# Optimization experiments

Measured on AMD Instinct MI355X. Metric: run time of the kernel, lower is better.

Reference implementation:

```python
import jax, jax.numpy as jnp
import numpy as np

B, L, C, H = 2, 4096, 512, 8
DH = C // H


def setup_inputs() -> dict:
    key = jax.random.key(0)
    ks = jax.random.split(key, 6)
    s = 1.0 / np.sqrt(C)
    return {
        "x": jax.random.normal(ks[0], (B, L, C), dtype=jnp.float32),
        "Wq": jax.random.normal(ks[1], (C, C), dtype=jnp.float32) * s,
        "Wk": jax.random.normal(ks[2], (C, C), dtype=jnp.float32) * s,
        "Wv": jax.random.normal(ks[3], (C, C), dtype=jnp.float32) * s,
        "Wo": jax.random.normal(ks[4], (C, C), dtype=jnp.float32) * s,
        "bo": jnp.zeros((C,), dtype=jnp.float32),
    }


def reference(x, Wq, Wk, Wv, Wo, bo):
    # x: [B, L, C]; split heads -> [B, H, L, Dh]
    def heads(t):
        return t.reshape(B, L, H, DH).transpose(0, 2, 1, 3)

    q = heads(x @ Wq)
    k = heads(x @ Wk)
    v = heads(x @ Wv)
    scale = 1.0 / np.sqrt(DH)
    scores = jnp.einsum("bhqd,bhkd->bhqk", q, k) * scale  # [B,H,L,L]
    w = jax.nn.softmax(scores, axis=-1)  # dropout_rate=0.0 -> identity
    att = jnp.einsum("bhqk,bhkd->bhqd", w, v)  # [B,H,L,Dh]
    att = att.transpose(0, 2, 1, 3).reshape(B, L, C)
    return att @ Wo + bo
```

## Files before the change

kernel.cpp:

```cpp
#include <hip/hip_runtime.h>
#include <hip/hip_bf16.h>

typedef __hip_bfloat16 bh;
typedef __attribute__((ext_vector_type(8))) __bf16 bf16x8;
typedef __attribute__((ext_vector_type(4))) float f32x4;
typedef __attribute__((ext_vector_type(4))) int i32x4;
typedef __attribute__((ext_vector_type(4))) short s16x4;

#define NB 2
#define NL 4096
#define NC 512
#define NH 8
#define NDH 64
#define NM (NB * NL)
#define LOG2E 1.4426950408889634f
#define KVBLK 8192

static __device__ __forceinline__ f32x4 mfma_bf16(bf16x8 a, bf16x8 b, f32x4 c) {
    return __builtin_amdgcn_mfma_f32_16x16x32_bf16(a, b, c, 0, 0, 0);
}

static __device__ __forceinline__ void st_bf4(bh* dst, float a, float b, float c, float d) {
    bh tmp[4] = {__float2bfloat16(a), __float2bfloat16(b),
                 __float2bfloat16(c), __float2bfloat16(d)};
    *(s16x4*)dst = *(const s16x4*)tmp;
}
static __device__ __forceinline__ bf16x8 pk_bf8(float a0, float a1, float a2, float a3,
                                                float b0, float b1, float b2, float b3) {
    bh tmp[8] = {__float2bfloat16(a0), __float2bfloat16(a1),
                 __float2bfloat16(a2), __float2bfloat16(a3),
                 __float2bfloat16(b0), __float2bfloat16(b1),
                 __float2bfloat16(b2), __float2bfloat16(b3)};
    return *(const bf16x8*)tmp;
}

static __device__ __forceinline__ void gload16(const bh* g, bh* l) {
    __builtin_amdgcn_global_load_lds(
        (const __attribute__((address_space(1))) void*)g,
        (__attribute__((address_space(3))) void*)l,
        16, 0, 0);
}

__global__ __launch_bounds__(256, 2)
void prep(const float* __restrict__ x,
          const float* __restrict__ Wq, const float* __restrict__ Wk,
          const float* __restrict__ Wv, const float* __restrict__ Wo,
          bh* __restrict__ xf, bh* __restrict__ Wf)
{
    const int t = threadIdx.x;
    const int wave = t >> 6, lane = t & 63;
    const int quad = lane >> 4, c16 = lane & 15;

    if (blockIdx.z < 8) {
        __shared__ __align__(16) bh T[64][72];
        const int m64 = blockIdx.x, k64 = blockIdx.z;
        #pragma unroll
        for (int rep = 0; rep < 4; rep++) {
            int li = t + rep * 256;
            int r = li >> 4, c4 = (li & 15) * 4;
            float4 f = *(const float4*)&x[(size_t)(m64 * 64 + r) * 512 + k64 * 64 + c4];
            st_bf4(&T[r][c4], f.x, f.y, f.z, f.w);
        }
        __syncthreads();
        #pragma unroll
        for (int kcl = 0; kcl < 2; kcl++) {
            i32x4 v = *(const i32x4*)&T[wave * 16 + c16][kcl * 32 + quad * 8];
            size_t addr = ((size_t)(m64 * 4 + wave) * 16 + (k64 * 2 + kcl)) * 512 + lane * 8;
            *(i32x4*)&xf[addr] = v;
        }
    } else {
        if (blockIdx.x >= 64) return;
        int task = blockIdx.x * 4 + wave;
        int z = task >> 6, nt = (task >> 3) & 7, k0i = task & 7;
        const float* W = (z == 0) ? Wq : (z == 1) ? Wk : (z == 2) ? Wv : Wo;
        bh* dst = Wf + (((size_t)z * 8 + nt) * 8 + k0i) * 4096;
        #pragma unroll
        for (int kc = 0; kc < 2; kc++)
            #pragma unroll
            for (int fn = 0; fn < 4; fn++) {
                bh tmp[8];
                #pragma unroll
                for (int j = 0; j < 8; j++)
                    tmp[j] = __float2bfloat16(
                        W[(size_t)(k0i * 64 + kc * 32 + quad * 8 + j) * 512
                          + nt * 64 + fn * 16 + c16]);
                *(i32x4*)&dst[(kc * 4 + fn) * 512 + lane * 8] = *(const i32x4*)tmp;
            }
    }
}

__global__ __launch_bounds__(256, 2)
void qkv_gemm(const bh* __restrict__ xf, const bh* __restrict__ Wf,
              bh* __restrict__ Qb, bh* __restrict__ KVf)
{
    __shared__ __align__(16) bh smem[2][20480];

    const int t = threadIdx.x;
    const int wave = t >> 6, lane = t & 63;
    const int quad = lane >> 4, c16 = lane & 15;
    const int m0 = blockIdx.x * 128;
    const int nt = blockIdx.y;
    const int m16b = m0 >> 4;

    f32x4 acc[3][2][4];
    for (int z = 0; z < 3; z++)
        for (int a = 0; a < 2; a++)
            for (int b = 0; b < 4; b++)
                for (int u = 0; u < 4; u++) acc[z][a][b][u] = 0.0f;

    auto stage = [&](int k0i, int buf) {
        bh* Xl = &smem[buf][0];
        bh* Wl = &smem[buf][8192];
        #pragma unroll
        for (int r = 0; r < 4; r++) {
            int f = wave * 4 + r;
            const bh* src = xf + ((size_t)(m16b + (f >> 1)) * 16 + k0i * 2 + (f & 1)) * 512
                          + lane * 8;
            gload16(src, &Xl[f * 512 + lane * 8]);
        }
        #pragma unroll
        for (int z = 0; z < 3; z++) {
            const bh* wz = Wf + (((size_t)z * 8 + nt) * 8 + k0i) * 4096;
            #pragma unroll
            for (int r = 0; r < 2; r++) {
                int off = (wave * 2 + r) * 512 + lane * 8;
                gload16(wz + off, &Wl[z * 4096 + off]);
            }
        }
    };

    stage(0, 0);
    for (int k0i = 0; k0i < 8; k0i++) {
        const int buf = k0i & 1;
        __syncthreads();
        if (k0i < 7) stage(k0i + 1, buf ^ 1);
        const bh* Xl = &smem[buf][0];
        const bh* Wl = &smem[buf][8192];
        #pragma unroll
        for (int kc = 0; kc < 2; kc++) {
            bf16x8 af0 = *(const bf16x8*)&Xl[((wave * 2 + 0) * 2 + kc) * 512 + lane * 8];
            bf16x8 af1 = *(const bf16x8*)&Xl[((wave * 2 + 1) * 2 + kc) * 512 + lane * 8];
            #pragma unroll
            for (int z = 0; z < 3; z++)
                #pragma unroll
                for (int fn = 0; fn < 4; fn++) {
                    bf16x8 bf = *(const bf16x8*)&Wl[z * 4096 + (kc * 4 + fn) * 512 + lane * 8];
                    acc[z][0][fn] = mfma_bf16(af0, bf, acc[z][0][fn]);
                    acc[z][1][fn] = mfma_bf16(af1, bf, acc[z][1][fn]);
                }
        }
        __syncthreads();
    }

    const int h = nt;
    const int b = m0 >> 12;
    const int l0 = m0 & 4095;
    const int bh_i = b * NH + h;
    const int kt0 = l0 >> 6;

    {
        bh* Tq = &smem[0][0];
        #pragma unroll
        for (int fm = 0; fm < 2; fm++)
            #pragma unroll
            for (int i = 0; i < 4; i++) {
                int ll = wave * 32 + fm * 16 + quad * 4 + i;
                #pragma unroll
                for (int fn = 0; fn < 4; fn++)
                    Tq[ll * 68 + fn * 16 + c16] =
                        __float2bfloat16(acc[0][fm][fn][i] * 0.125f);
            }
        __syncthreads();
        int l = t >> 1, half = t & 1;
        bh* dst = Qb + ((size_t)bh_i * NL + l0 + l) * NDH + half * 32;
        const bh* src = &Tq[l * 68 + half * 32];
        #pragma unroll
        for (int r = 0; r < 4; r++)
            *(i32x4*)(dst + r * 8) = *(const i32x4*)(src + r * 8);
        __syncthreads();
    }

    {
        bh* Tk = &smem[0][0];
        #pragma unroll
        for (int fm = 0; fm < 2; fm++)
            #pragma unroll
            for (int i = 0; i < 4; i++) {
                int ll = wave * 32 + fm * 16 + quad * 4 + i;
                int ktl = ll >> 6, l64 = ll & 63;
                int fk = l64 >> 4, c16t = l64 & 15;
                #pragma unroll
                for (int fn = 0; fn < 4; fn++) {
                    int d = fn * 16 + c16;
                    int kc = d >> 5, qt = (d >> 3) & 3, j = d & 7;
                    Tk[ktl * 4096 + (fk * 2 + kc) * 512 + (qt * 16 + c16t) * 8 + j] =
                        __float2bfloat16(acc[1][fm][fn][i] * LOG2E);
                }
            }
        __syncthreads();
        int idx = t * 32;
        int ktl = idx >> 12, wi = idx & 4095;
        bh* dst = KVf + (size_t)(bh_i * 64 + kt0 + ktl) * KVBLK + wi;
        #pragma unroll
        for (int r = 0; r < 4; r++)
            *(i32x4*)(dst + r * 8) = *(const i32x4*)&Tk[idx + r * 8];
    }

    #pragma unroll
    for (int fm = 0; fm < 2; fm++) {
        int fkv = (wave * 2 + fm) & 3;
        int ktv = kt0 + (wave >> 1);
        #pragma unroll
        for (int fn = 0; fn < 4; fn++) {
            size_t addr = (size_t)(bh_i * 64 + ktv) * KVBLK + 4096
                        + (size_t)(fn * 2 + (fkv >> 1)) * 512 + lane * 8 + (fkv & 1) * 4;
            st_bf4(&KVf[addr], acc[2][fm][fn][0], acc[2][fm][fn][1],
                               acc[2][fm][fn][2], acc[2][fm][fn][3]);
        }
    }
}

__global__ __launch_bounds__(512, 4)
void flash_attn(const bh* __restrict__ Qb, const bh* __restrict__ KVf,
                bh* __restrict__ attb)
{
    __shared__ __align__(16) bh SF[2][2][KVBLK];

    const int t = threadIdx.x;
    const int wave = t >> 6, lane = t & 63;
    const int group = wave >> 2, w4 = wave & 3;
    const int quad = lane >> 4, c16 = lane & 15;

    const int bid = blockIdx.x + blockIdx.y * 32;
    const int work = (bid & 7) * 64 + (bid >> 3);
    const int bh_idx = work >> 5;
    const int q0 = (work & 31) * 128;

    const bh* Qp  = Qb + (size_t)bh_idx * NL * NDH;
    const bh* KVp = KVf + (size_t)bh_idx * 64 * KVBLK;

    bf16x8 qf[2][2];
    #pragma unroll
    for (int fq = 0; fq < 2; fq++)
        #pragma unroll
        for (int kc = 0; kc < 2; kc++)
            qf[fq][kc] = *(const bf16x8*)
                &Qp[(size_t)(q0 + w4 * 32 + fq * 16 + c16) * NDH + kc * 32 + quad * 8];

    f32x4 ot[4][2];
    float lsum[2] = {0.0f, 0.0f};
    for (int a = 0; a < 4; a++)
        for (int fq = 0; fq < 2; fq++)
            for (int u = 0; u < 4; u++) ot[a][fq][u] = 0.0f;
    const f32x4 z4 = {0.0f, 0.0f, 0.0f, 0.0f};

    auto stage = [&](int i, int buf) {
        int kt = 2 * i + group;
        #pragma unroll
        for (int r = 0; r < 4; r++) {
            int off = (w4 * 4 + r) * 512 + lane * 8;
            gload16(KVp + (size_t)kt * KVBLK + off, &SF[group][buf][off]);
        }
    };

    stage(0, 0);
    for (int i = 0; i < 32; i++) {
        const int buf = i & 1;
        __syncthreads();
        if (i < 31) stage(i + 1, buf ^ 1);
        const bh* sf = &SF[group][buf][0];

        f32x4 s[4][2];
        #pragma unroll
        for (int fk = 0; fk < 4; fk++) {
            bf16x8 kf0 = *(const bf16x8*)&sf[(fk * 2 + 0) * 512 + lane * 8];
            s[fk][0] = mfma_bf16(kf0, qf[0][0], z4);
            s[fk][1] = mfma_bf16(kf0, qf[1][0], z4);
        }
        #pragma unroll
        for (int fk = 0; fk < 4; fk++) {
            bf16x8 kf1 = *(const bf16x8*)&sf[(fk * 2 + 1) * 512 + lane * 8];
            s[fk][0] = mfma_bf16(kf1, qf[0][1], s[fk][0]);
            s[fk][1] = mfma_bf16(kf1, qf[1][1], s[fk][1]);
        }

        bf16x8 vt[4][2];
        #pragma unroll
        for (int fn = 0; fn < 4; fn++)
            #pragma unroll
            for (int a = 0; a < 2; a++)
                vt[fn][a] = *(const bf16x8*)&sf[4096 + (fn * 2 + a) * 512 + lane * 8];

        float rs0 = 0.0f, rs1 = 0.0f;
        #pragma unroll
        for (int a = 0; a < 2; a++) {
            float a0 = __builtin_amdgcn_exp2f(s[2 * a][0][0]);
            float a1 = __builtin_amdgcn_exp2f(s[2 * a][0][1]);
            float a2 = __builtin_amdgcn_exp2f(s[2 * a][0][2]);
            float a3 = __builtin_amdgcn_exp2f(s[2 * a][0][3]);
            float a4 = __builtin_amdgcn_exp2f(s[2 * a + 1][0][0]);
            float a5 = __builtin_amdgcn_exp2f(s[2 * a + 1][0][1]);
            float a6 = __builtin_amdgcn_exp2f(s[2 * a + 1][0][2]);
            float a7 = __builtin_amdgcn_exp2f(s[2 * a + 1][0][3]);
            rs0 += ((a0 + a1) + (a2 + a3)) + ((a4 + a5) + (a6 + a7));
            bf16x8 p0 = pk_bf8(a0, a1, a2, a3, a4, a5, a6, a7);
            float b0 = __builtin_amdgcn_exp2f(s[2 * a][1][0]);
            float b1 = __builtin_amdgcn_exp2f(s[2 * a][1][1]);
            float b2 = __builtin_amdgcn_exp2f(s[2 * a][1][2]);
            float b3 = __builtin_amdgcn_exp2f(s[2 * a][1][3]);
            float b4 = __builtin_amdgcn_exp2f(s[2 * a + 1][1][0]);
            float b5 = __builtin_amdgcn_exp2f(s[2 * a + 1][1][1]);
            float b6 = __builtin_amdgcn_exp2f(s[2 * a + 1][1][2]);
            float b7 = __builtin_amdgcn_exp2f(s[2 * a + 1][1][3]);
            rs1 += ((b0 + b1) + (b2 + b3)) + ((b4 + b5) + (b6 + b7));
            bf16x8 p1 = pk_bf8(b0, b1, b2, b3, b4, b5, b6, b7);
            #pragma unroll
            for (int fn = 0; fn < 4; fn++) {
                ot[fn][0] = mfma_bf16(vt[fn][a], p0, ot[fn][0]);
                ot[fn][1] = mfma_bf16(vt[fn][a], p1, ot[fn][1]);
            }
        }
        lsum[0] += rs0;
        lsum[1] += rs1;
    }

    #pragma unroll
    for (int fq = 0; fq < 2; fq++) {
        lsum[fq] += __shfl_xor(lsum[fq], 16);
        lsum[fq] += __shfl_xor(lsum[fq], 32);
    }

    float* Ocmb = (float*)&SF[0][0][0];
    float* Lcmb = Ocmb + 128 * 64;
    __syncthreads();
    if (group == 1) {
        #pragma unroll
        for (int fq = 0; fq < 2; fq++) {
            int q = w4 * 32 + fq * 16 + c16;
            #pragma unroll
            for (int fn = 0; fn < 4; fn++)
                *(f32x4*)&Ocmb[q * 64 + fn * 16 + quad * 4] = ot[fn][fq];
            if (quad == 0) Lcmb[q] = lsum[fq];
        }
    }
    __syncthreads();
    if (group == 0) {
        const int b = bh_idx >> 3, h = bh_idx & 7;
        const int mbase16 = (b * NL + q0) >> 4;
        #pragma unroll
        for (int fq = 0; fq < 2; fq++) {
            int q = w4 * 32 + fq * 16 + c16;
            float inv = 1.0f / (lsum[fq] + Lcmb[q]);
            int m16 = mbase16 + w4 * 2 + fq;
            #pragma unroll
            for (int fn = 0; fn < 4; fn++) {
                f32x4 o2 = *(const f32x4*)&Ocmb[q * 64 + fn * 16 + quad * 4];
                size_t addr = ((size_t)m16 * 16 + h * 2 + (fn >> 1)) * 512
                            + (size_t)(((fn & 1) * 2 + (quad >> 1)) * 16 + c16) * 8
                            + (quad & 1) * 4;
                st_bf4(&attb[addr],
                       (ot[fn][fq][0] + o2[0]) * inv, (ot[fn][fq][1] + o2[1]) * inv,
                       (ot[fn][fq][2] + o2[2]) * inv, (ot[fn][fq][3] + o2[3]) * inv);
            }
        }
    }
}

__global__ __launch_bounds__(256, 2)
void out_gemm(const bh* __restrict__ Af, const bh* __restrict__ Wf,
              const float* __restrict__ bo, float* __restrict__ out)
{
    __shared__ __align__(16) bh smem[2][12288];

    const int t = threadIdx.x;
    const int wave = t >> 6, lane = t & 63;
    const int quad = lane >> 4, c16 = lane & 15;
    const int m0 = blockIdx.x * 128;
    const int nt = blockIdx.y;
    const int n0 = nt * 64;
    const int m16b = m0 >> 4;

    f32x4 acc[2][4];
    for (int a = 0; a < 2; a++)
        for (int b = 0; b < 4; b++)
            for (int u = 0; u < 4; u++) acc[a][b][u] = 0.0f;

    auto stage = [&](int k0i, int buf) {
        bh* Xl = &smem[buf][0];
        bh* Wl = &smem[buf][8192];
        #pragma unroll
        for (int r = 0; r < 4; r++) {
            int f = wave * 4 + r;
            const bh* src = Af + ((size_t)(m16b + (f >> 1)) * 16 + k0i * 2 + (f & 1)) * 512
                          + lane * 8;
            gload16(src, &Xl[f * 512 + lane * 8]);
        }
        const bh* wz = Wf + (((size_t)3 * 8 + nt) * 8 + k0i) * 4096;
        #pragma unroll
        for (int r = 0; r < 2; r++) {
            int off = (wave * 2 + r) * 512 + lane * 8;
            gload16(wz + off, &Wl[off]);
        }
    };

    stage(0, 0);
    for (int k0i = 0; k0i < 8; k0i++) {
        const int buf = k0i & 1;
        __syncthreads();
        if (k0i < 7) stage(k0i + 1, buf ^ 1);
        const bh* Xl = &smem[buf][0];
        const bh* Wl = &smem[buf][8192];
        #pragma unroll
        for (int kc = 0; kc < 2; kc++) {
            bf16x8 af0 = *(const bf16x8*)&Xl[((wave * 2 + 0) * 2 + kc) * 512 + lane * 8];
            bf16x8 af1 = *(const bf16x8*)&Xl[((wave * 2 + 1) * 2 + kc) * 512 + lane * 8];
            #pragma unroll
            for (int fn = 0; fn < 4; fn++) {
                bf16x8 bf = *(const bf16x8*)&Wl[(kc * 4 + fn) * 512 + lane * 8];
                acc[0][fn] = mfma_bf16(af0, bf, acc[0][fn]);
                acc[1][fn] = mfma_bf16(af1, bf, acc[1][fn]);
            }
        }
        __syncthreads();
    }

    #pragma unroll
    for (int fm = 0; fm < 2; fm++)
        #pragma unroll
        for (int i = 0; i < 4; i++) {
            int mr = m0 + wave * 32 + fm * 16 + quad * 4 + i;
            #pragma unroll
            for (int fn = 0; fn < 4; fn++) {
                int cn = n0 + fn * 16 + c16;
                out[(size_t)mr * 512 + cn] = acc[fm][fn][i] + bo[cn];
            }
        }
}

extern "C" void kernel_launch(void* const* d_in, const int* in_sizes, int n_in,
                              void* d_out, int out_size, void* d_ws, size_t ws_size,
                              hipStream_t stream)
{
    const float* x  = (const float*)d_in[0];
    const float* Wq = (const float*)d_in[1];
    const float* Wk = (const float*)d_in[2];
    const float* Wv = (const float*)d_in[3];
    const float* Wo = (const float*)d_in[4];
    const float* bo = (const float*)d_in[5];
    float* out = (float*)d_out;

    const size_t mat = (size_t)NM * NC;
    bh* Qb   = (bh*)d_ws;
    bh* KVf  = Qb + mat;
    bh* attb = KVf + 2 * mat;
    bh* Wf   = attb + mat;
    bh* xf   = Wf + 4 * 8 * 8 * 4096;

    prep      <<<dim3(128, 1, 9),         256, 0, stream>>>(x, Wq, Wk, Wv, Wo, xf, Wf);
    qkv_gemm  <<<dim3(NM / 128, NC / 64), 256, 0, stream>>>(xf, Wf, Qb, KVf);
    flash_attn<<<dim3(NL / 128, NB * NH), 512, 0, stream>>>(Qb, KVf, attb);
    out_gemm  <<<dim3(NM / 128, NC / 64), 256, 0, stream>>>(attb, Wf, bo, out);
}
```

Measured before the change: 178.1 us.

## Halve M-tile and K-step in projection GEMMs to raise block count and occupancy

Both the QKV and output projection GEMMs move from 128-row tiles with a 64-wide K step to 64-row tiles with a 32-wide K step. This doubles the grid and shrinks shared memory and registers per block, and launch bounds now allow 4 blocks per CU. The epilogue layout math is redone for the smaller tile. The aim is better CU fill on a 256-CU part, at the cost of less operand reuse and twice as many barrier-separated K iterations. The out_gemm loop also drops its trailing syncthreads.

After: 178.6 us. About the same (+0.3%).

```diff
diff --git a/kernel.cpp b/kernel.cpp
--- a/kernel.cpp
+++ b/kernel.cpp
@@ -89,68 +89,54 @@
     }
 }
 
-__global__ __launch_bounds__(256, 2)
+__global__ __launch_bounds__(256, 4)
 void qkv_gemm(const bh* __restrict__ xf, const bh* __restrict__ Wf,
               bh* __restrict__ Qb, bh* __restrict__ KVf)
 {
-    __shared__ __align__(16) bh smem[2][20480];
+    __shared__ __align__(16) bh smem[2][8192];
 
     const int t = threadIdx.x;
     const int wave = t >> 6, lane = t & 63;
     const int quad = lane >> 4, c16 = lane & 15;
-    const int m0 = blockIdx.x * 128;
+    const int m0 = blockIdx.x * 64;
     const int nt = blockIdx.y;
     const int m16b = m0 >> 4;
 
-    f32x4 acc[3][2][4];
+    f32x4 acc[3][4];
     for (int z = 0; z < 3; z++)
-        for (int a = 0; a < 2; a++)
-            for (int b = 0; b < 4; b++)
-                for (int u = 0; u < 4; u++) acc[z][a][b][u] = 0.0f;
-
-    auto stage = [&](int k0i, int buf) {
+        for (int fn = 0; fn < 4; fn++)
+            for (int u = 0; u < 4; u++) acc[z][fn][u] = 0.0f;
+
+    auto stage = [&](int k32, int buf) {
         bh* Xl = &smem[buf][0];
-        bh* Wl = &smem[buf][8192];
-        #pragma unroll
-        for (int r = 0; r < 4; r++) {
-            int f = wave * 4 + r;
-            const bh* src = xf + ((size_t)(m16b + (f >> 1)) * 16 + k0i * 2 + (f & 1)) * 512
-                          + lane * 8;
-            gload16(src, &Xl[f * 512 + lane * 8]);
-        }
+        bh* Wl = &smem[buf][2048];
+        gload16(xf + ((size_t)(m16b + wave) * 16 + k32) * 512 + lane * 8,
+                &Xl[wave * 512 + lane * 8]);
         #pragma unroll
         for (int z = 0; z < 3; z++) {
-            const bh* wz = Wf + (((size_t)z * 8 + nt) * 8 + k0i) * 4096;
-            #pragma unroll
-            for (int r = 0; r < 2; r++) {
-                int off = (wave * 2 + r) * 512 + lane * 8;
-                gload16(wz + off, &Wl[z * 4096 + off]);
+            const bh* wz = Wf + (((size_t)z * 8 + nt) * 8 + (k32 >> 1)) * 4096
+                         + (size_t)((k32 & 1) * 4 + wave) * 512;
+            gload16(wz + lane * 8, &Wl[z * 2048 + wave * 512 + lane * 8]);
+        }
+    };
+
+    stage(0, 0);
+    for (int k32 = 0; k32 < 16; k32++) {
+        const int buf = k32 & 1;
+        __syncthreads();
+        if (k32 < 15) stage(k32 + 1, buf ^ 1);
+        const bh* Xl = &smem[buf][0];
+        const bh* Wl = &smem[buf][2048];
+        bf16x8 af = *(const bf16x8*)&Xl[wave * 512 + lane * 8];
+        #pragma unroll
+        for (int z = 0; z < 3; z++)
+            #pragma unroll
+            for (int fn = 0; fn < 4; fn++) {
+                bf16x8 bf = *(const bf16x8*)&Wl[z * 2048 + fn * 512 + lane * 8];
+                acc[z][fn] = mfma_bf16(af, bf, acc[z][fn]);
             }
-        }
-    };
-
-    stage(0, 0);
-    for (int k0i = 0; k0i < 8; k0i++) {
-        const int buf = k0i & 1;
-        __syncthreads();
-        if (k0i < 7) stage(k0i + 1, buf ^ 1);
-        const bh* Xl = &smem[buf][0];
-        const bh* Wl = &smem[buf][8192];
-        #pragma unroll
-        for (int kc = 0; kc < 2; kc++) {
-            bf16x8 af0 = *(const bf16x8*)&Xl[((wave * 2 + 0) * 2 + kc) * 512 + lane * 8];
-            bf16x8 af1 = *(const bf16x8*)&Xl[((wave * 2 + 1) * 2 + kc) * 512 + lane * 8];
-            #pragma unroll
-            for (int z = 0; z < 3; z++)
-                #pragma unroll
-                for (int fn = 0; fn < 4; fn++) {
-                    bf16x8 bf = *(const bf16x8*)&Wl[z * 4096 + (kc * 4 + fn) * 512 + lane * 8];
-                    acc[z][0][fn] = mfma_bf16(af0, bf, acc[z][0][fn]);
-                    acc[z][1][fn] = mfma_bf16(af1, bf, acc[z][1][fn]);
-                }
-        }
-        __syncthreads();
-    }
+    }
+    __syncthreads();
 
     const int h = nt;
     const int b = m0 >> 12;
@@ -161,62 +147,48 @@
     {
         bh* Tq = &smem[0][0];
         #pragma unroll
-        for (int fm = 0; fm < 2; fm++)
-            #pragma unroll
-            for (int i = 0; i < 4; i++) {
-                int ll = wave * 32 + fm * 16 + quad * 4 + i;
-                #pragma unroll
-                for (int fn = 0; fn < 4; fn++)
-                    Tq[ll * 68 + fn * 16 + c16] =
-                        __float2bfloat16(acc[0][fm][fn][i] * 0.125f);
-            }
-        __syncthreads();
-        int l = t >> 1, half = t & 1;
-        bh* dst = Qb + ((size_t)bh_i * NL + l0 + l) * NDH + half * 32;
-        const bh* src = &Tq[l * 68 + half * 32];
-        #pragma unroll
-        for (int r = 0; r < 4; r++)
-            *(i32x4*)(dst + r * 8) = *(const i32x4*)(src + r * 8);
+        for (int i = 0; i < 4; i++) {
+            int ll = wave * 16 + quad * 4 + i;
+            #pragma unroll
+            for (int fn = 0; fn < 4; fn++)
+                Tq[ll * 68 + fn * 16 + c16] =
+                    __float2bfloat16(acc[0][fn][i] * 0.125f);
+        }
+        __syncthreads();
+        int l = t >> 2, part = t & 3;
+        bh* dst = Qb + ((size_t)bh_i * NL + l0 + l) * NDH + part * 16;
+        const bh* src = &Tq[l * 68 + part * 16];
+        *(i32x4*)(dst)     = *(const i32x4*)(src);
+        *(i32x4*)(dst + 8) = *(const i32x4*)(src + 8);
         __syncthreads();
     }
 
     {
         bh* Tk = &smem[0][0];
         #pragma unroll
-        for (int fm = 0; fm < 2; fm++)
-            #pragma unroll
-            for (int i = 0; i < 4; i++) {
-                int ll = wave * 32 + fm * 16 + quad * 4 + i;
-                int ktl = ll >> 6, l64 = ll & 63;
-                int fk = l64 >> 4, c16t = l64 & 15;
-                #pragma unroll
-                for (int fn = 0; fn < 4; fn++) {
-                    int d = fn * 16 + c16;
-                    int kc = d >> 5, qt = (d >> 3) & 3, j = d & 7;
-                    Tk[ktl * 4096 + (fk * 2 + kc) * 512 + (qt * 16 + c16t) * 8 + j] =
-                        __float2bfloat16(acc[1][fm][fn][i] * LOG2E);
-                }
+        for (int i = 0; i < 4; i++) {
+            int c16t = quad * 4 + i;
+            #pragma unroll
+            for (int fn = 0; fn < 4; fn++) {
+                int d = fn * 16 + c16;
+                int kc = d >> 5, qt = (d >> 3) & 3, j = d & 7;
+                Tk[(wave * 2 + kc) * 512 + (qt * 16 + c16t) * 8 + j] =
+                    __float2bfloat16(acc[1][fn][i] * LOG2E);
             }
-        __syncthreads();
-        int idx = t * 32;
-        int ktl = idx >> 12, wi = idx & 4095;
-        bh* dst = KVf + (size_t)(bh_i * 64 + kt0 + ktl) * KVBLK + wi;
-        #pragma unroll
-        for (int r = 0; r < 4; r++)
-            *(i32x4*)(dst + r * 8) = *(const i32x4*)&Tk[idx + r * 8];
+        }
+        __syncthreads();
+        int idx = t * 16;
+        bh* dst = KVf + (size_t)(bh_i * 64 + kt0) * KVBLK + idx;
+        *(i32x4*)(dst)     = *(const i32x4*)&Tk[idx];
+        *(i32x4*)(dst + 8) = *(const i32x4*)&Tk[idx + 8];
     }
 
     #pragma unroll
-    for (int fm = 0; fm < 2; fm++) {
-        int fkv = (wave * 2 + fm) & 3;
-        int ktv = kt0 + (wave >> 1);
-        #pragma unroll
-        for (int fn = 0; fn < 4; fn++) {
-            size_t addr = (size_t)(bh_i * 64 + ktv) * KVBLK + 4096
-                        + (size_t)(fn * 2 + (fkv >> 1)) * 512 + lane * 8 + (fkv & 1) * 4;
-            st_bf4(&KVf[addr], acc[2][fm][fn][0], acc[2][fm][fn][1],
-                               acc[2][fm][fn][2], acc[2][fm][fn][3]);
-        }
+    for (int fn = 0; fn < 4; fn++) {
+        size_t addr = (size_t)(bh_i * 64 + kt0) * KVBLK + 4096
+                    + (size_t)(fn * 2 + (wave >> 1)) * 512 + lane * 8 + (wave & 1) * 4;
+        st_bf4(&KVf[addr], acc[2][fn][0], acc[2][fn][1],
+                           acc[2][fn][2], acc[2][fn][3]);
     }
 }
 
@@ -366,75 +338,58 @@
     }
 }
 
-__global__ __launch_bounds__(256, 2)
+__global__ __launch_bounds__(256, 4)
 void out_gemm(const bh* __restrict__ Af, const bh* __restrict__ Wf,
               const float* __restrict__ bo, float* __restrict__ out)
 {
-    __shared__ __align__(16) bh smem[2][12288];
+    __shared__ __align__(16) bh smem[2][4096];
 
     const int t = threadIdx.x;
     const int wave = t >> 6, lane = t & 63;
     const int quad = lane >> 4, c16 = lane & 15;
-    const int m0 = blockIdx.x * 128;
+    const int m0 = blockIdx.x * 64;
     const int nt = blockIdx.y;
     const int n0 = nt * 64;
     const int m16b = m0 >> 4;
 
-    f32x4 acc[2][4];
-    for (int a = 0; a < 2; a++)
-        for (int b = 0; b < 4; b++)
-            for (int u = 0; u < 4; u++) acc[a][b][u] = 0.0f;
-
-    auto stage = [&](int k0i, int buf) {
+    f32x4 acc[4];
+    for (int fn = 0; fn < 4; fn++)
+        for (int u = 0; u < 4; u++) acc[fn][u] = 0.0f;
+
+    auto stage = [&](int k32, int buf) {
         bh* Xl = &smem[buf][0];
-        bh* Wl = &smem[buf][8192];
-        #pragma unroll
-        for (int r = 0; r < 4; r++) {
-            int f = wave * 4 + r;
-            const bh* src = Af + ((size_t)(m16b + (f >> 1)) * 16 + k0i * 2 + (f & 1)) * 512
-                          + lane * 8;
-            gload16(src, &Xl[f * 512 + lane * 8]);
-        }
-        const bh* wz = Wf + (((size_t)3 * 8 + nt) * 8 + k0i) * 4096;
-        #pragma unroll
-        for (int r = 0; r < 2; r++) {
-            int off = (wave * 2 + r) * 512 + lane * 8;
-            gload16(wz + off, &Wl[off]);
-        }
+        bh* Wl = &smem[buf][2048];
+        gload16(Af + ((size_t)(m16b + wave) * 16 + k32) * 512 + lane * 8,
+                &Xl[wave * 512 + lane * 8]);
+        const bh* wz = Wf + (((size_t)3 * 8 + nt) * 8 + (k32 >> 1)) * 4096
+                     + (size_t)((k32 & 1) * 4 + wave) * 512;
+        gload16(wz + lane * 8, &Wl[wave * 512 + lane * 8]);
     };
 
     stage(0, 0);
-    for (int k0i = 0; k0i < 8; k0i++) {
-        const int buf = k0i & 1;
-        __syncthreads();
-        if (k0i < 7) stage(k0i + 1, buf ^ 1);
+    for (int k32 = 0; k32 < 16; k32++) {
+        const int buf = k32 & 1;
+        __syncthreads();
+        if (k32 < 15) stage(k32 + 1, buf ^ 1);
         const bh* Xl = &smem[buf][0];
-        const bh* Wl = &smem[buf][8192];
-        #pragma unroll
-        for (int kc = 0; kc < 2; kc++) {
-            bf16x8 af0 = *(const bf16x8*)&Xl[((wave * 2 + 0) * 2 + kc) * 512 + lane * 8];
-            bf16x8 af1 = *(const bf16x8*)&Xl[((wave * 2 + 1) * 2 + kc) * 512 + lane * 8];
-            #pragma unroll
-            for (int fn = 0; fn < 4; fn++) {
-                bf16x8 bf = *(const bf16x8*)&Wl[(kc * 4 + fn) * 512 + lane * 8];
-                acc[0][fn] = mfma_bf16(af0, bf, acc[0][fn]);
-                acc[1][fn] = mfma_bf16(af1, bf, acc[1][fn]);
-            }
-        }
-        __syncthreads();
+        const bh* Wl = &smem[buf][2048];
+        bf16x8 af = *(const bf16x8*)&Xl[wave * 512 + lane * 8];
+        #pragma unroll
+        for (int fn = 0; fn < 4; fn++) {
+            bf16x8 bf = *(const bf16x8*)&Wl[fn * 512 + lane * 8];
+            acc[fn] = mfma_bf16(af, bf, acc[fn]);
+        }
     }
 
     #pragma unroll
-    for (int fm = 0; fm < 2; fm++)
-        #pragma unroll
-        for (int i = 0; i < 4; i++) {
-            int mr = m0 + wave * 32 + fm * 16 + quad * 4 + i;
-            #pragma unroll
-            for (int fn = 0; fn < 4; fn++) {
-                int cn = n0 + fn * 16 + c16;
-                out[(size_t)mr * 512 + cn] = acc[fm][fn][i] + bo[cn];
-            }
-        }
+    for (int i = 0; i < 4; i++) {
+        int mr = m0 + wave * 16 + quad * 4 + i;
+        #pragma unroll
+        for (int fn = 0; fn < 4; fn++) {
+            int cn = n0 + fn * 16 + c16;
+            out[(size_t)mr * 512 + cn] = acc[fn][i] + bo[cn];
+        }
+    }
 }
 
 extern "C" void kernel_launch(void* const* d_in, const int* in_sizes, int n_in,
@@ -457,7 +412,7 @@
     bh* xf   = Wf + 4 * 8 * 8 * 4096;
 
     prep      <<<dim3(128, 1, 9),         256, 0, stream>>>(x, Wq, Wk, Wv, Wo, xf, Wf);
-    qkv_gemm  <<<dim3(NM / 128, NC / 64), 256, 0, stream>>>(xf, Wf, Qb, KVf);
+    qkv_gemm  <<<dim3(NM / 64, NC / 64),  256, 0, stream>>>(xf, Wf, Qb, KVf);
     flash_attn<<<dim3(NL / 128, NB * NH), 512, 0, stream>>>(Qb, KVf, attb);
-    out_gemm  <<<dim3(NM / 128, NC / 64), 256, 0, stream>>>(attb, Wf, bo, out);
-}
+    out_gemm  <<<dim3(NM / 64, NC / 64),  256, 0, stream>>>(attb, Wf, bo, out);
+}
```
